# Kernel tuning notes

Hardware: AMD Instinct MI355X
Metric: run time of the kernel (lower is better)

## Reference

```python
import jax, jax.numpy as jnp
import numpy as np

N = 100000      # nodes
E = 1600000     # edges (avg degree 16)
DIN, DH, DOUT = 256, 128, 64
EPS = 1e-5      # BatchNorm eps


def setup_inputs() -> dict:
    key = jax.random.key(0)
    ks = jax.random.split(key, 8)
    x = jax.random.normal(ks[0], (N, DIN), dtype=jnp.float32)
    edge_index = jax.random.randint(ks[1], (2, E), 0, N, dtype=jnp.int32)
    # Glorot-ish scaled weights
    W1 = jax.random.normal(ks[2], (DIN, DH), jnp.float32) * (1.0 / np.sqrt(DIN))
    W2 = jax.random.normal(ks[3], (DH, DH), jnp.float32) * (1.0 / np.sqrt(DH))
    W3 = jax.random.normal(ks[4], (DH, DOUT), jnp.float32) * (1.0 / np.sqrt(DH))
    return {
        "x": x, "edge_index": edge_index,
        "W1": W1, "b1": jnp.zeros((DH,), jnp.float32),
        "g1": jnp.ones((DH,), jnp.float32), "bt1": jnp.zeros((DH,), jnp.float32),
        "W2": W2, "b2": jnp.zeros((DH,), jnp.float32),
        "g2": jnp.ones((DH,), jnp.float32), "bt2": jnp.zeros((DH,), jnp.float32),
        "W3": W3, "b3": jnp.zeros((DOUT,), jnp.float32),
    }


def reference(x, edge_index, W1, b1, g1, bt1, W2, b2, g2, bt2, W3, b3):
    n = x.shape[0]
    src, dst = edge_index[0], edge_index[1]
    # GCNConv default: add self-loops, symmetric normalization D^-1/2 (A+I) D^-1/2
    loop = jnp.arange(n, dtype=edge_index.dtype)
    s = jnp.concatenate([src, loop])   # [E+N]
    d = jnp.concatenate([dst, loop])
    deg = jax.ops.segment_sum(jnp.ones_like(s, dtype=x.dtype), d, num_segments=n)
    dinv = jax.lax.rsqrt(deg)          # deg >= 1 due to self-loops
    norm = dinv[s] * dinv[d]           # [E+N]

    def conv(h, W, b):
        h = h @ W                                  # transform then propagate
        msg = h[s] * norm[:, None]                 # gather + scale
        return jax.ops.segment_sum(msg, d, num_segments=n) + b  # scatter-add

    def bn(h, g, bt):                              # training-mode BatchNorm1d
        mu = h.mean(0)
        var = ((h - mu) ** 2).mean(0)              # biased variance
        return g * (h - mu) * jax.lax.rsqrt(var + EPS) + bt

    h = jax.nn.relu(bn(conv(x, W1, b1), g1, bt1))
    h = jax.nn.relu(bn(conv(h, W2, b2), g2, bt2))
    return conv(h, W3, b3)
```

## Files before the change

### kernel.cpp

```cpp
#include <hip/hip_runtime.h>
#include <hip/hip_bf16.h>

#define DEVINL __device__ __forceinline__

constexpr int NN   = 100000;
constexpr int NE   = 1600000;
constexpr int DIN  = 256;
constexpr int DH   = 128;
constexpr int DOUT = 64;
constexpr float BN_EPS = 1e-5f;
constexpr int NBUCK = (NN + 127) / 128;
constexpr int CHUNK = 8192;
constexpr int NBF   = (NE + CHUNK - 1) / CHUNK;
constexpr int SORT_CAP = 4096;

typedef __attribute__((ext_vector_type(8))) short short8;
typedef __attribute__((ext_vector_type(4))) float f32x4;

DEVINL ushort f2bf(float f) {
  uint u = __builtin_bit_cast(uint, f);
  u += 0x7FFFu + ((u >> 16) & 1u);
  return (ushort)(u >> 16);
}
DEVINL float bf2f(ushort u) {
  return __builtin_bit_cast(float, ((uint)u) << 16);
}


__launch_bounds__(256)
__global__ void k_bhist(const int* __restrict__ dst, int* __restrict__ bcnt) {
  __shared__ int h[NBUCK];
  const int t = threadIdx.x;
  for (int i = t; i < NBUCK; i += 256) h[i] = 0;
  __syncthreads();
  const int e00 = blockIdx.x * 4096;
  for (int k = 0; k < 16; ++k) {
    int e = e00 + k * 256 + t;
    if (e < NE) atomicAdd(&h[dst[e] >> 7], 1);
  }
  __syncthreads();
  for (int i = t; i < NBUCK; i += 256)
    if (h[i]) atomicAdd(&bcnt[i], h[i]);
}

__global__ void k_bscan(const int* __restrict__ bcnt, int* __restrict__ boffs,
                        int* __restrict__ gcursor) {
  __shared__ int s[1024];
  const int t = threadIdx.x;
  int v = (t < NBUCK) ? bcnt[t] : 0;
  int x = v;
  s[t] = x; __syncthreads();
  for (int off = 1; off < 1024; off <<= 1) {
    int y = (t >= off) ? s[t - off] : 0;
    __syncthreads();
    x += y; s[t] = x;
    __syncthreads();
  }
  if (t < NBUCK) { boffs[t] = x - v; gcursor[t] = x - v; }
  if (t == 0) boffs[NBUCK] = NE;
}

__launch_bounds__(256)
__global__ void k_bfill(const int* __restrict__ src, const int* __restrict__ dst,
                        int* __restrict__ gcursor, uint* __restrict__ ebuf) {
  __shared__ uint   sortv[CHUNK];
  __shared__ ushort sortb[CHUNK];
  __shared__ int hist[NBUCK];
  __shared__ int start[NBUCK];
  __shared__ int gbase[NBUCK];
  const int t = threadIdx.x;
  const int e00 = blockIdx.x * CHUNK;
  const int nv = min(CHUNK, NE - e00);

  for (int i = t; i < NBUCK; i += 256) hist[i] = 0;
  __syncthreads();
  for (int k = 0; k < CHUNK / 256; ++k) {
    int e = e00 + k * 256 + t;
    if (e < NE) atomicAdd(&hist[dst[e] >> 7], 1);
  }
  __syncthreads();

  int c[4]; int sl = 0;
#pragma unroll
  for (int j = 0; j < 4; ++j) {
    int b = t * 4 + j;
    c[j] = (b < NBUCK) ? hist[b] : 0;
    sl += c[j];
  }
  gbase[t] = sl;
  __syncthreads();
  int x = sl;
  for (int off = 1; off < 256; off <<= 1) {
    int y = (t >= off) ? gbase[t - off] : 0;
    __syncthreads();
    x += y; gbase[t] = x;
    __syncthreads();
  }
  int run = x - sl;
#pragma unroll
  for (int j = 0; j < 4; ++j) {
    int b = t * 4 + j;
    if (b < NBUCK) start[b] = run;
    run += c[j];
  }
  __syncthreads();

  for (int i = t; i < NBUCK; i += 256) {
    int cnt = hist[i];
    if (cnt > 0) gbase[i] = atomicAdd(&gcursor[i], cnt);
    hist[i] = start[i];
  }
  __syncthreads();

  for (int k = 0; k < CHUNK / 256; ++k) {
    int e = e00 + k * 256 + t;
    if (e < NE) {
      int d = dst[e];
      int b = d >> 7;
      int r = atomicAdd(&hist[b], 1);
      sortv[r] = (uint)src[e] | ((uint)(d & 127) << 17);
      sortb[r] = (ushort)b;
    }
  }
  __syncthreads();

  for (int i = t; i < nv; i += 256) {
    int b = sortb[i];
    ebuf[gbase[b] + (i - start[b])] = sortv[i];
  }
}

__launch_bounds__(256)
__global__ void k_sort(uint* __restrict__ ebuf, const int* __restrict__ boffs,
                       int* __restrict__ offs, float* __restrict__ dinv) {
  __shared__ uint vals[SORT_CAP];
  __shared__ int cnt[128], pre[128], cur[128];
  const int t = threadIdx.x;
  const int b = blockIdx.x;
  const int e0 = boffs[b];
  const int e1 = boffs[b + 1];
  const int n = e1 - e0;

  if (t < 128) cnt[t] = 0;
  __syncthreads();
  for (int i = t; i < n; i += 256) {
    uint v = ebuf[e0 + i];
    vals[i] = v;
    atomicAdd(&cnt[v >> 17], 1);
  }
  __syncthreads();

  if (t < 128) pre[t] = cnt[t];
  __syncthreads();
  for (int off = 1; off < 128; off <<= 1) {
    int y = (t < 128 && t >= off) ? pre[t - off] : 0;
    __syncthreads();
    if (t < 128) pre[t] += y;
    __syncthreads();
  }
  if (t < 128) {
    const int excl = pre[t] - cnt[t];
    cur[t] = excl;
    const int nid = b * 128 + t;
    if (nid < NN) {
      offs[nid] = e0 + excl;
      dinv[nid] = rsqrtf((float)cnt[t] + 1.0f);
    } else if (nid == NN) {
      offs[NN] = e0 + excl;
    }
  }
  __syncthreads();

  for (int i = t; i < n; i += 256) {
    const uint v = vals[i];
    const int r = atomicAdd(&cur[v >> 17], 1);
    ebuf[e0 + r] = v & 0x1FFFFu;
  }
}

__global__ void k_pack(const float* __restrict__ W, ushort* __restrict__ Wp, int K, int Nw) {
  int t = blockIdx.x * 256 + threadIdx.x;
  int total = (K / 32) * (Nw / 16) * 64;
  if (t >= total) return;
  int l  = t & 63;
  int nf = (t >> 6) % (Nw / 16);
  int ks = (t >> 6) / (Nw / 16);
  int krow = ks * 32 + (l >> 4) * 8;
  int col  = nf * 16 + (l & 15);
  ushort out[8];
#pragma unroll
  for (int j = 0; j < 8; ++j) out[j] = f2bf(W[(size_t)(krow + j) * Nw + col]);
  *(uint4*)&Wp[(size_t)t * 8] = *(const uint4*)out;
}

template <int K, int NW, bool BN>
__launch_bounds__(256)
__global__ void k_gemm(const float* __restrict__ A, const ushort* __restrict__ Wp,
                       const float* __restrict__ scale, const float* __restrict__ shift,
                       const float* __restrict__ dinv, ushort* __restrict__ Cout, int M) {
  constexpr int LDA = 40;
  __shared__ ushort lds[128 * LDA];
  const int t = threadIdx.x;
  const int lane = t & 63;
  const int wid = t >> 6;
  const int m0 = blockIdx.x * 128;

  constexpr int WAVES_N = (NW == 128) ? 2 : 1;
  constexpr int MF  = (NW == 128) ? 4 : 2;
  constexpr int NFW = 4;
  constexpr int NFT = NW / 16;
  const int wr = wid / WAVES_N;
  const int wc = wid % WAVES_N;
  const int mbase = wr * (MF * 16);
  const int nfg0 = wc * NFW;

  f32x4 acc[MF][NFW] = {};

  const int cg = t & 7;
  const int r0 = t >> 3;

  const int nkt = K / 32;
  for (int kt = 0; kt < nkt; ++kt) {
    const int k0 = kt * 32;
    float4 s4 = {1.f, 1.f, 1.f, 1.f}, h4 = {0.f, 0.f, 0.f, 0.f};
    if (BN) {
      s4 = *(const float4*)&scale[k0 + cg * 4];
      h4 = *(const float4*)&shift[k0 + cg * 4];
    }
    __syncthreads();
#pragma unroll
    for (int p = 0; p < 4; ++p) {
      const int row = p * 32 + r0;
      const int grow = m0 + row;
      float4 v = {0.f, 0.f, 0.f, 0.f};
      if (grow < M) v = *(const float4*)&A[(size_t)grow * K + k0 + cg * 4];
      if (BN) {
        v.x = fmaxf(v.x * s4.x + h4.x, 0.f);
        v.y = fmaxf(v.y * s4.y + h4.y, 0.f);
        v.z = fmaxf(v.z * s4.z + h4.z, 0.f);
        v.w = fmaxf(v.w * s4.w + h4.w, 0.f);
      }
      ushort4 w;
      w.x = f2bf(v.x); w.y = f2bf(v.y); w.z = f2bf(v.z); w.w = f2bf(v.w);
      *(ushort4*)&lds[row * LDA + cg * 4] = w;
    }
    __syncthreads();

    short8 bfrag[NFW];
#pragma unroll
    for (int nf = 0; nf < NFW; ++nf) {
      const size_t bidx = ((size_t)(kt * NFT + nfg0 + nf) * 64 + lane) * 8;
      bfrag[nf] = *(const short8*)&Wp[bidx];
    }
#pragma unroll
    for (int mf = 0; mf < MF; ++mf) {
      const short8 af =
          *(const short8*)&lds[(mbase + mf * 16 + (lane & 15)) * LDA + ((lane >> 4) * 8)];
#pragma unroll
      for (int nf = 0; nf < NFW; ++nf)
        acc[mf][nf] = __builtin_amdgcn_mfma_f32_16x16x32_bf16(af, bfrag[nf], acc[mf][nf], 0, 0, 0);
    }
  }

#pragma unroll
  for (int mf = 0; mf < MF; ++mf) {
#pragma unroll
    for (int r = 0; r < 4; ++r) {
      const int grow = m0 + mbase + mf * 16 + (lane >> 4) * 4 + r;
      if (grow < M) {
        const float dv = dinv[grow];
#pragma unroll
        for (int nf = 0; nf < NFW; ++nf) {
          const int gcol = (nfg0 + nf) * 16 + (lane & 15);
          Cout[(size_t)grow * NW + gcol] = f2bf(acc[mf][nf][r] * dv);
        }
      }
    }
  }
}

__launch_bounds__(256)
__global__ void k_prop128(const ushort* __restrict__ G, const int* __restrict__ offs,
                          const int* __restrict__ csr, const float* __restrict__ dinv,
                          const float* __restrict__ bias, float* __restrict__ H, int n) {
  const int wid = threadIdx.x >> 6;
  const int lane = threadIdx.x & 63;
  const int nid = blockIdx.x * 4 + wid;
  if (nid >= n) return;
  const int d0 = lane * 2;
  const size_t base = (size_t)nid * 128;
  ushort2 gs = *(const ushort2*)&G[base + d0];
  float a0 = bf2f(gs.x);
  float a1 = bf2f(gs.y);
  const int e0 = offs[nid];
  const int e1 = offs[nid + 1];
  for (int e = e0; e < e1; e += 8) {
    int idx[8];
#pragma unroll
    for (int i = 0; i < 8; ++i) idx[i] = (e + i < e1) ? csr[e + i] : nid;
    ushort2 g[8];
#pragma unroll
    for (int i = 0; i < 8; ++i) g[i] = *(const ushort2*)&G[(size_t)idx[i] * 128 + d0];
#pragma unroll
    for (int i = 0; i < 8; ++i) {
      if (e + i < e1) {
        a0 += bf2f(g[i].x);
        a1 += bf2f(g[i].y);
      }
    }
  }
  const float di = dinv[nid];
  const float2 b2 = *(const float2*)&bias[d0];
  float2 o;
  o.x = a0 * di + b2.x;
  o.y = a1 * di + b2.y;
  *(float2*)&H[base + d0] = o;
}

__launch_bounds__(256)
__global__ void k_prop64(const ushort* __restrict__ G, const int* __restrict__ offs,
                         const int* __restrict__ csr, const float* __restrict__ dinv,
                         const float* __restrict__ bias, float* __restrict__ out, int n) {
  const int wid = threadIdx.x >> 6;
  const int lane = threadIdx.x & 63;
  const int nid = blockIdx.x * 4 + wid;
  if (nid >= n) return;
  float a = bf2f(G[(size_t)nid * 64 + lane]);
  const int e0 = offs[nid];
  const int e1 = offs[nid + 1];
  for (int e = e0; e < e1; e += 8) {
    int idx[8];
#pragma unroll
    for (int i = 0; i < 8; ++i) idx[i] = (e + i < e1) ? csr[e + i] : nid;
    ushort g[8];
#pragma unroll
    for (int i = 0; i < 8; ++i) g[i] = G[(size_t)idx[i] * 64 + lane];
#pragma unroll
    for (int i = 0; i < 8; ++i)
      if (e + i < e1) a += bf2f(g[i]);
  }
  out[(size_t)nid * 64 + lane] = a * dinv[nid] + bias[lane];
}

__launch_bounds__(256)
__global__ void k_stats(const float* __restrict__ H, float* __restrict__ sum,
                        float* __restrict__ sumsq, int n) {
  const int d = threadIdx.x & 127;
  const int half = threadIdx.x >> 7;
  const int rpb = (n + gridDim.x - 1) / gridDim.x;
  const int r0 = blockIdx.x * rpb;
  const int r1 = min(n, r0 + rpb);
  float s = 0.f, q = 0.f;
  for (int r = r0 + half; r < r1; r += 2) {
    const float v = H[(size_t)r * 128 + d];
    s += v;
    q += v * v;
  }
  __shared__ float ls[256], lq[256];
  ls[threadIdx.x] = s;
  lq[threadIdx.x] = q;
  __syncthreads();
  if (half == 0) {
    atomicAdd(&sum[d], s + ls[d + 128]);
    atomicAdd(&sumsq[d], q + lq[d + 128]);
  }
}

__global__ void k_finalize(const float* __restrict__ sum, const float* __restrict__ sumsq,
                           const float* __restrict__ g, const float* __restrict__ bt,
                           float* __restrict__ scale, float* __restrict__ shift) {
  const int d = threadIdx.x;
  const float inv_n = 1.0f / (float)NN;
  const float mu = sum[d] * inv_n;
  float var = sumsq[d] * inv_n - mu * mu;
  const float rs = rsqrtf(var + BN_EPS);
  const float sc = g[d] * rs;
  scale[d] = sc;
  shift[d] = bt[d] - mu * sc;
}

extern "C" void kernel_launch(void* const* d_in, const int* in_sizes, int n_in,
                              void* d_out, int out_size, void* d_ws, size_t ws_size,
                              hipStream_t stream) {
  const float* x   = (const float*)d_in[0];
  const int*  ei   = (const int*)d_in[1];
  const int*  srcp = ei;
  const int*  dstp = ei + NE;
  const float* W1  = (const float*)d_in[2];
  const float* b1  = (const float*)d_in[3];
  const float* g1  = (const float*)d_in[4];
  const float* bt1 = (const float*)d_in[5];
  const float* W2  = (const float*)d_in[6];
  const float* b2  = (const float*)d_in[7];
  const float* g2  = (const float*)d_in[8];
  const float* bt2 = (const float*)d_in[9];
  const float* W3  = (const float*)d_in[10];
  const float* b3  = (const float*)d_in[11];
  float* out = (float*)d_out;

  char* p = (char*)d_ws;
  auto alloc = [&](size_t bytes) {
    char* r = p;
    p += (bytes + 255) & ~(size_t)255;
    return r;
  };
  int*    bcnt    = (int*)alloc(NBUCK * 4);
  int*    boffs   = (int*)alloc((NBUCK + 1) * 4);
  int*    gcursor = (int*)alloc(NBUCK * 4);
  uint*   ebuf    = (uint*)alloc((size_t)NE * 4);
  int*    offs    = (int*)alloc((NN + 1) * 4);
  float*  dinv    = (float*)alloc(NN * 4);
  float*  gsum    = (float*)alloc(DH * 4);
  float*  gsumsq  = (float*)alloc(DH * 4);
  float*  scale   = (float*)alloc(DH * 4);
  float*  shift   = (float*)alloc(DH * 4);
  ushort* Wp1     = (ushort*)alloc((size_t)DIN * DH * 2);
  ushort* Wp2     = (ushort*)alloc((size_t)DH * DH * 2);
  ushort* Wp3     = (ushort*)alloc((size_t)DH * DOUT * 2);
  ushort* G       = (ushort*)alloc((size_t)NN * DH * 2);
  float*  H       = (float*)alloc((size_t)NN * DH * 4);

  const int GB = (NN + 127) / 128;
  const int PB = (NN + 3) / 4;

  hipMemsetAsync(bcnt, 0, NBUCK * 4, stream);
  k_bhist<<<(NE + 4095) / 4096, 256, 0, stream>>>(dstp, bcnt);
  k_bscan<<<1, 1024, 0, stream>>>(bcnt, boffs, gcursor);
  k_bfill<<<NBF, 256, 0, stream>>>(srcp, dstp, gcursor, ebuf);
  k_sort<<<NBUCK, 256, 0, stream>>>(ebuf, boffs, offs, dinv);
  const int* csr = (const int*)ebuf;

  k_pack<<<16, 256, 0, stream>>>(W1, Wp1, DIN, DH);
  k_pack<<<8, 256, 0, stream>>>(W2, Wp2, DH, DH);
  k_pack<<<4, 256, 0, stream>>>(W3, Wp3, DH, DOUT);

  k_gemm<DIN, DH, false><<<GB, 256, 0, stream>>>(x, Wp1, nullptr, nullptr, dinv, G, NN);
  k_prop128<<<PB, 256, 0, stream>>>(G, offs, csr, dinv, b1, H, NN);
  hipMemsetAsync(gsum, 0, DH * 4, stream);
  hipMemsetAsync(gsumsq, 0, DH * 4, stream);
  k_stats<<<512, 256, 0, stream>>>(H, gsum, gsumsq, NN);
  k_finalize<<<1, DH, 0, stream>>>(gsum, gsumsq, g1, bt1, scale, shift);

  k_gemm<DH, DH, true><<<GB, 256, 0, stream>>>(H, Wp2, scale, shift, dinv, G, NN);
  k_prop128<<<PB, 256, 0, stream>>>(G, offs, csr, dinv, b2, H, NN);
  hipMemsetAsync(gsum, 0, DH * 4, stream);
  hipMemsetAsync(gsumsq, 0, DH * 4, stream);
  k_stats<<<512, 256, 0, stream>>>(H, gsum, gsumsq, NN);
  k_finalize<<<1, DH, 0, stream>>>(gsum, gsumsq, g2, bt2, scale, shift);

  k_gemm<DH, DOUT, true><<<GB, 256, 0, stream>>>(H, Wp3, scale, shift, dinv, G, NN);
  k_prop64<<<PB, 256, 0, stream>>>(G, offs, csr, dinv, b3, out, NN);
}
```

Baseline: 608.9 us.

## Fuse BatchNorm statistics into propagation and widen gather to 8-byte loads

The 128-wide propagation kernel becomes a persistent grid-stride kernel. Each wave splits its edges between two half-waves that each load 4 bf16 features per lane, and the halves are combined with a cross-lane shuffle. Per-feature sum and sum-of-squares are accumulated in registers and reduced once per block with atomics, which removes the separate stats pass that re-read H. The 64-wide propagation gets the same treatment, with four quarter-waves each loading 4 features. This trades extra shuffles and partially idle lanes for fewer, wider gather loads and one less full pass over H.

```diff
diff --git a/kernel.cpp b/kernel.cpp
--- a/kernel.cpp
+++ b/kernel.cpp
@@ -279,42 +279,92 @@
   }
 }
 
+template <bool STATS>
 __launch_bounds__(256)
 __global__ void k_prop128(const ushort* __restrict__ G, const int* __restrict__ offs,
                           const int* __restrict__ csr, const float* __restrict__ dinv,
-                          const float* __restrict__ bias, float* __restrict__ H, int n) {
-  const int wid = threadIdx.x >> 6;
-  const int lane = threadIdx.x & 63;
-  const int nid = blockIdx.x * 4 + wid;
-  if (nid >= n) return;
-  const int d0 = lane * 2;
-  const size_t base = (size_t)nid * 128;
-  ushort2 gs = *(const ushort2*)&G[base + d0];
-  float a0 = bf2f(gs.x);
-  float a1 = bf2f(gs.y);
-  const int e0 = offs[nid];
-  const int e1 = offs[nid + 1];
-  for (int e = e0; e < e1; e += 8) {
-    int idx[8];
-#pragma unroll
-    for (int i = 0; i < 8; ++i) idx[i] = (e + i < e1) ? csr[e + i] : nid;
-    ushort2 g[8];
-#pragma unroll
-    for (int i = 0; i < 8; ++i) g[i] = *(const ushort2*)&G[(size_t)idx[i] * 128 + d0];
-#pragma unroll
-    for (int i = 0; i < 8; ++i) {
-      if (e + i < e1) {
-        a0 += bf2f(g[i].x);
-        a1 += bf2f(g[i].y);
-      }
-    }
-  }
-  const float di = dinv[nid];
-  const float2 b2 = *(const float2*)&bias[d0];
-  float2 o;
-  o.x = a0 * di + b2.x;
-  o.y = a1 * di + b2.y;
-  *(float2*)&H[base + d0] = o;
+                          const float* __restrict__ bias, float* __restrict__ H,
+                          float* __restrict__ gsum, float* __restrict__ gsumsq) {
+  const int t = threadIdx.x;
+  const int wid = t >> 6;
+  const int lane = t & 63;
+  const int h = lane >> 5;
+  const int li = lane & 31;
+  const int f0 = li * 4;
+
+  float s0 = 0.f, s1 = 0.f, s2 = 0.f, s3 = 0.f;
+  float q0 = 0.f, q1 = 0.f, q2 = 0.f, q3 = 0.f;
+
+  const int stride = gridDim.x * 4;
+  for (int nid = blockIdx.x * 4 + wid; nid < NN; nid += stride) {
+    float a0 = 0.f, a1 = 0.f, a2 = 0.f, a3 = 0.f;
+    if (h == 0) {
+      ushort4 gs = *(const ushort4*)&G[(size_t)nid * 128 + f0];
+      a0 = bf2f(gs.x); a1 = bf2f(gs.y); a2 = bf2f(gs.z); a3 = bf2f(gs.w);
+    }
+    const int e0 = offs[nid];
+    const int e1 = offs[nid + 1];
+    for (int e = e0; e < e1; e += 16) {
+      int idx[8];
+#pragma unroll
+      for (int j = 0; j < 8; ++j) {
+        const int ei = e + 2 * j + h;
+        idx[j] = (ei < e1) ? csr[ei] : nid;
+      }
+      ushort4 g[8];
+#pragma unroll
+      for (int j = 0; j < 8; ++j)
+        g[j] = *(const ushort4*)&G[(size_t)idx[j] * 128 + f0];
+#pragma unroll
+      for (int j = 0; j < 8; ++j) {
+        const int ei = e + 2 * j + h;
+        if (ei < e1) {
+          a0 += bf2f(g[j].x); a1 += bf2f(g[j].y);
+          a2 += bf2f(g[j].z); a3 += bf2f(g[j].w);
+        }
+      }
+    }
+    a0 += __shfl_xor(a0, 32, 64);
+    a1 += __shfl_xor(a1, 32, 64);
+    a2 += __shfl_xor(a2, 32, 64);
+    a3 += __shfl_xor(a3, 32, 64);
+    if (h == 0) {
+      const float di = dinv[nid];
+      const float4 b4 = *(const float4*)&bias[f0];
+      float4 o;
+      o.x = a0 * di + b4.x; o.y = a1 * di + b4.y;
+      o.z = a2 * di + b4.z; o.w = a3 * di + b4.w;
+      *(float4*)&H[(size_t)nid * 128 + f0] = o;
+      if (STATS) {
+        s0 += o.x; s1 += o.y; s2 += o.z; s3 += o.w;
+        q0 += o.x * o.x; q1 += o.y * o.y; q2 += o.z * o.z; q3 += o.w * o.w;
+      }
+    }
+  }
+
+  if (STATS) {
+    __shared__ float ls[4][32][4];
+    __shared__ float lq[4][32][4];
+    if (h == 0) {
+      ls[wid][li][0] = s0; ls[wid][li][1] = s1; ls[wid][li][2] = s2; ls[wid][li][3] = s3;
+      lq[wid][li][0] = q0; lq[wid][li][1] = q1; lq[wid][li][2] = q2; lq[wid][li][3] = q3;
+    }
+    __syncthreads();
+    if (t < 32) {
+#pragma unroll
+      for (int k = 0; k < 4; ++k) {
+        float v = ls[0][t][k] + ls[1][t][k] + ls[2][t][k] + ls[3][t][k];
+        atomicAdd(&gsum[t * 4 + k], v);
+      }
+    } else if (t < 64) {
+      const int u = t - 32;
+#pragma unroll
+      for (int k = 0; k < 4; ++k) {
+        float v = lq[0][u][k] + lq[1][u][k] + lq[2][u][k] + lq[3][u][k];
+        atomicAdd(&gsumsq[u * 4 + k], v);
+      }
+    }
+  }
 }
 
 __launch_bounds__(256)
@@ -325,44 +375,48 @@
   const int lane = threadIdx.x & 63;
   const int nid = blockIdx.x * 4 + wid;
   if (nid >= n) return;
-  float a = bf2f(G[(size_t)nid * 64 + lane]);
+  const int q = lane >> 4;
+  const int li = lane & 15;
+  const int f0 = li * 4;
+
+  float a0 = 0.f, a1 = 0.f, a2 = 0.f, a3 = 0.f;
+  if (q == 0) {
+    ushort4 gs = *(const ushort4*)&G[(size_t)nid * 64 + f0];
+    a0 = bf2f(gs.x); a1 = bf2f(gs.y); a2 = bf2f(gs.z); a3 = bf2f(gs.w);
+  }
   const int e0 = offs[nid];
   const int e1 = offs[nid + 1];
-  for (int e = e0; e < e1; e += 8) {
-    int idx[8];
-#pragma unroll
-    for (int i = 0; i < 8; ++i) idx[i] = (e + i < e1) ? csr[e + i] : nid;
-    ushort g[8];
-#pragma unroll
-    for (int i = 0; i < 8; ++i) g[i] = G[(size_t)idx[i] * 64 + lane];
-#pragma unroll
-    for (int i = 0; i < 8; ++i)
-      if (e + i < e1) a += bf2f(g[i]);
-  }
-  out[(size_t)nid * 64 + lane] = a * dinv[nid] + bias[lane];
-}
-
-__launch_bounds__(256)
-__global__ void k_stats(const float* __restrict__ H, float* __restrict__ sum,
-                        float* __restrict__ sumsq, int n) {
-  const int d = threadIdx.x & 127;
-  const int half = threadIdx.x >> 7;
-  const int rpb = (n + gridDim.x - 1) / gridDim.x;
-  const int r0 = blockIdx.x * rpb;
-  const int r1 = min(n, r0 + rpb);
-  float s = 0.f, q = 0.f;
-  for (int r = r0 + half; r < r1; r += 2) {
-    const float v = H[(size_t)r * 128 + d];
-    s += v;
-    q += v * v;
-  }
-  __shared__ float ls[256], lq[256];
-  ls[threadIdx.x] = s;
-  lq[threadIdx.x] = q;
-  __syncthreads();
-  if (half == 0) {
-    atomicAdd(&sum[d], s + ls[d + 128]);
-    atomicAdd(&sumsq[d], q + lq[d + 128]);
+  for (int e = e0; e < e1; e += 16) {
+    int idx[4];
+#pragma unroll
+    for (int j = 0; j < 4; ++j) {
+      const int ei = e + 4 * j + q;
+      idx[j] = (ei < e1) ? csr[ei] : nid;
+    }
+    ushort4 g[4];
+#pragma unroll
+    for (int j = 0; j < 4; ++j)
+      g[j] = *(const ushort4*)&G[(size_t)idx[j] * 64 + f0];
+#pragma unroll
+    for (int j = 0; j < 4; ++j) {
+      const int ei = e + 4 * j + q;
+      if (ei < e1) {
+        a0 += bf2f(g[j].x); a1 += bf2f(g[j].y);
+        a2 += bf2f(g[j].z); a3 += bf2f(g[j].w);
+      }
+    }
+  }
+  a0 += __shfl_xor(a0, 16, 64); a1 += __shfl_xor(a1, 16, 64);
+  a2 += __shfl_xor(a2, 16, 64); a3 += __shfl_xor(a3, 16, 64);
+  a0 += __shfl_xor(a0, 32, 64); a1 += __shfl_xor(a1, 32, 64);
+  a2 += __shfl_xor(a2, 32, 64); a3 += __shfl_xor(a3, 32, 64);
+  if (lane < 16) {
+    const float di = dinv[nid];
+    const float4 b4 = *(const float4*)&bias[f0];
+    float4 o;
+    o.x = a0 * di + b4.x; o.y = a1 * di + b4.y;
+    o.z = a2 * di + b4.z; o.w = a3 * di + b4.w;
+    *(float4*)&out[(size_t)nid * 64 + f0] = o;
   }
 }
 
@@ -422,6 +476,7 @@
 
   const int GB = (NN + 127) / 128;
   const int PB = (NN + 3) / 4;
+  const int SB = 2048;
 
   hipMemsetAsync(bcnt, 0, NBUCK * 4, stream);
   k_bhist<<<(NE + 4095) / 4096, 256, 0, stream>>>(dstp, bcnt);
@@ -435,17 +490,15 @@
   k_pack<<<4, 256, 0, stream>>>(W3, Wp3, DH, DOUT);
 
   k_gemm<DIN, DH, false><<<GB, 256, 0, stream>>>(x, Wp1, nullptr, nullptr, dinv, G, NN);
-  k_prop128<<<PB, 256, 0, stream>>>(G, offs, csr, dinv, b1, H, NN);
   hipMemsetAsync(gsum, 0, DH * 4, stream);
   hipMemsetAsync(gsumsq, 0, DH * 4, stream);
-  k_stats<<<512, 256, 0, stream>>>(H, gsum, gsumsq, NN);
+  k_prop128<true><<<SB, 256, 0, stream>>>(G, offs, csr, dinv, b1, H, gsum, gsumsq);
   k_finalize<<<1, DH, 0, stream>>>(gsum, gsumsq, g1, bt1, scale, shift);
 
   k_gemm<DH, DH, true><<<GB, 256, 0, stream>>>(H, Wp2, scale, shift, dinv, G, NN);
-  k_prop128<<<PB, 256, 0, stream>>>(G, offs, csr, dinv, b2, H, NN);
   hipMemsetAsync(gsum, 0, DH * 4, stream);
   hipMemsetAsync(gsumsq, 0, DH * 4, stream);
-  k_stats<<<512, 256, 0, stream>>>(H, gsum, gsumsq, NN);
+  k_prop128<true><<<SB, 256, 0, stream>>>(G, offs, csr, dinv, b2, H, gsum, gsumsq);
   k_finalize<<<1, DH, 0, stream>>>(gsum, gsumsq, g2, bt2, scale, shift);
 
   k_gemm<DH, DOUT, true><<<GB, 256, 0, stream>>>(H, Wp3, scale, shift, dinv, G, NN);
```

Result: slower. 888.4 us (+45.9%).
